# Kernel optimization log

Hardware: AMD Instinct MI355X
Metric: run time of the kernel (lower is better)

## Reference

```python
import jax, jax.numpy as jnp
import numpy as np
from math import pi as PI

N = 50000       # nodes
E = 625000      # edges
G = 64          # graphs in batch
H = 128         # hidden_channels
FLT = 128       # num_filters
NG = 50         # num_gaussians
L = 6           # num_layers
CUTOFF = 10.0
LOG2 = float(np.log(2.0))


def ssp(x):
    # ShiftedSoftplus
    return jax.nn.softplus(x) - LOG2


def setup_inputs() -> dict:
    key = jax.random.key(0)
    ks = jax.random.split(key, 20)
    xav = lambda k, shp: jax.random.normal(k, shp, jnp.float32) * jnp.sqrt(2.0 / (shp[-2] + shp[-1]))
    inp = {
        "z": jax.random.randint(ks[0], (N,), 0, 100),
        "pos": jax.random.normal(ks[1], (N, 3), jnp.float32),
        "batch": jnp.sort(jax.random.randint(ks[2], (N,), 0, G)),
        "edge_index": jax.random.randint(ks[3], (2, E), 0, N),
        "emb_table": jax.random.normal(ks[4], (100, H), jnp.float32),
        # per-layer stacked params, Linear stored as (in, out)
        "lin_W": xav(ks[5], (L, H, FLT)),
        "mlp_W1": xav(ks[6], (L, NG, FLT)),
        "mlp_b1": jnp.zeros((L, FLT), jnp.float32),
        "mlp_W2": xav(ks[7], (L, FLT, FLT)),
        "mlp_b2": jnp.zeros((L, FLT), jnp.float32),
        "v_W1": xav(ks[8], (L, FLT, H)),
        "v_b1": jnp.zeros((L, H), jnp.float32),
        "v_W2": xav(ks[9], (L, H, H)),
        "v_b2": jnp.zeros((L, H), jnp.float32),
        "u_W1": xav(ks[10], (H, H // 2)),
        "u_b1": jnp.zeros((H // 2,), jnp.float32),
        "u_W2": xav(ks[11], (H // 2, 1)),
        "u_b2": jnp.zeros((1,), jnp.float32),
    }
    return inp


def reference(z, pos, batch, edge_index, emb_table, lin_W, mlp_W1, mlp_b1,
              mlp_W2, mlp_b2, v_W1, v_b1, v_W2, v_b2, u_W1, u_b1, u_W2, u_b2):
    row, col = edge_index[0], edge_index[1]  # (j, i)
    dist = jnp.linalg.norm(pos[row] - pos[col], axis=-1)  # [E]

    # gaussian distance embedding
    offset = jnp.linspace(0.0, CUTOFF, NG)
    coeff = -0.5 / (offset[1] - offset[0]) ** 2
    dist_emb = jnp.exp(coeff * (dist[:, None] - offset[None, :]) ** 2)  # [E, NG]

    # cosine cutoff
    C = 0.5 * (jnp.cos(dist * (PI / CUTOFF)) + 1.0)  # [E]

    v = emb_table[z]  # [N, H]
    for l in range(L):
        # update_e
        W = ssp(dist_emb @ mlp_W1[l] + mlp_b1[l]) @ mlp_W2[l] + mlp_b2[l]
        W = W * C[:, None]                       # [E, F]
        e = (v @ lin_W[l])[row] * W              # gather v[j], filter multiply
        # update_v
        agg = jax.ops.segment_sum(e, col, num_segments=N)  # scatter-add to i
        out = ssp(agg @ v_W1[l] + v_b1[l]) @ v_W2[l] + v_b2[l]
        v = v + out

    # update_u readout
    h = ssp(v @ u_W1 + u_b1) @ u_W2 + u_b2       # [N, 1]
    u = jax.ops.segment_sum(h, batch, num_segments=G)  # [G, 1]
    return u
```

## Files before the change

kernel.cpp:

```cpp
#include <hip/hip_runtime.h>
#include <math.h>

#define H 128
#define NG 50
#define TB 4096
#define DMAX 12.0f
#define LOG2F_ 0.69314718055994531f

typedef __attribute__((ext_vector_type(8))) short bfrag8;
typedef __attribute__((ext_vector_type(4))) float f32x4;
typedef __attribute__((ext_vector_type(8))) unsigned short u16x8;

__device__ __forceinline__ float sspf(float x) {
    float xc = fminf(x, 60.f);
    float r = __logf(1.f + __expf(xc)) - LOG2F_;
    return r + fmaxf(x - 60.f, 0.f);
}
__device__ __forceinline__ float bf2f(unsigned short u) {
    union { unsigned int i; float f; } c; c.i = ((unsigned int)u) << 16; return c.f;
}
__device__ __forceinline__ unsigned short f2bf(float f) {
    union { float f; unsigned int i; } c; c.f = f;
    unsigned int r = c.i + 0x7fffu + ((c.i >> 16) & 1u);
    return (unsigned short)(r >> 16);
}

__global__ void embed_kernel(const int* __restrict__ z, const float* __restrict__ emb,
                             unsigned short* __restrict__ vb, int n) {
    int idx = blockIdx.x * 256 + threadIdx.x;
    if (idx < n * H) {
        int node = idx >> 7, h = idx & 127;
        vb[idx] = f2bf(emb[z[node] * H + h]);
    }
}

__global__ void prep_w_kernel(const float* __restrict__ linW, const float* __restrict__ vW1,
                              const float* __restrict__ vW2, unsigned short* __restrict__ Wt) {
    int mat = blockIdx.x >> 4;
    int local = (blockIdx.x & 15) * 256 + threadIdx.x;
    int nrow = local >> 5;
    int k4 = local & 31;
    const float* src = (mat < 6) ? linW + mat * 16384
                     : (mat < 12) ? vW1 + (mat - 6) * 16384
                                  : vW2 + (mat - 12) * 16384;
    ushort4 o;
    o.x = f2bf(src[(k4 * 4 + 0) * H + nrow]);
    o.y = f2bf(src[(k4 * 4 + 1) * H + nrow]);
    o.z = f2bf(src[(k4 * 4 + 2) * H + nrow]);
    o.w = f2bf(src[(k4 * 4 + 3) * H + nrow]);
    *(ushort4*)(Wt + mat * 16384 + nrow * H + k4 * 4) = o;
}

__global__ void prep_u_kernel(const float* __restrict__ uW1, unsigned short* __restrict__ Ut) {
    int idx = blockIdx.x * 256 + threadIdx.x;
    int c = idx >> 7, k = idx & 127;
    Ut[c * H + k] = f2bf(uW1[k * 64 + c]);
}

__global__ void edge_dist_kernel(const int* __restrict__ ei, const float* __restrict__ pos,
                                 float* __restrict__ et, int* __restrict__ deg,
                                 int E_, float inv_step) {
    int e = blockIdx.x * 256 + threadIdx.x;
    if (e >= E_) return;
    int j = ei[e];
    int i = ei[E_ + e];
    float dx = pos[j*3+0] - pos[i*3+0];
    float dy = pos[j*3+1] - pos[i*3+1];
    float dz = pos[j*3+2] - pos[i*3+2];
    float d = sqrtf(dx*dx + dy*dy + dz*dz);
    float t = d * inv_step;
    t = fminf(t, (float)(TB - 2) + 0.9999f);
    et[e] = t;
    atomicAdd(&deg[i], 1);
}

__global__ void scanA_kernel(const int* __restrict__ deg, int* __restrict__ bsum, int n) {
    __shared__ int ws[16];
    int tid = threadIdx.x;
    int idx = blockIdx.x * 1024 + tid;
    int x = (idx < n) ? deg[idx] : 0;
    #pragma unroll
    for (int off = 32; off > 0; off >>= 1) x += __shfl_xor(x, off, 64);
    int lane = tid & 63, wid = tid >> 6;
    if (lane == 0) ws[wid] = x;
    __syncthreads();
    if (tid == 0) {
        int s = 0;
        #pragma unroll
        for (int i = 0; i < 16; ++i) s += ws[i];
        bsum[blockIdx.x] = s;
    }
}

__global__ void scanB_kernel(int* __restrict__ bsum, int nb) {
    int t = threadIdx.x;
    int x = (t < nb) ? bsum[t] : 0;
    int v = x;
    #pragma unroll
    for (int off = 1; off < 64; off <<= 1) {
        int y = __shfl_up(v, off, 64);
        if (t >= off) v += y;
    }
    if (t < nb) bsum[t] = v - x;
}

__global__ void scanC_kernel(const int* __restrict__ deg, const int* __restrict__ bsum,
                             int* __restrict__ row_ptr, int* __restrict__ cursor, int n) {
    __shared__ int wsum[16];
    int tid = threadIdx.x;
    int idx = blockIdx.x * 1024 + tid;
    int lane = tid & 63, wid = tid >> 6;
    int x = (idx < n) ? deg[idx] : 0;
    int v = x;
    #pragma unroll
    for (int off = 1; off < 64; off <<= 1) {
        int y = __shfl_up(v, off, 64);
        if (lane >= off) v += y;
    }
    if (lane == 63) wsum[wid] = v;
    __syncthreads();
    int woff = 0;
    for (int w = 0; w < wid; ++w) woff += wsum[w];
    int excl = bsum[blockIdx.x] + woff + v - x;
    if (idx < n) { row_ptr[idx] = excl; cursor[idx] = excl; }
    if (idx == n - 1) row_ptr[n] = excl + x;
}

__global__ void csr_fill_kernel(const int* __restrict__ ei, const float* __restrict__ et,
                                int* __restrict__ cursor, int* __restrict__ esrc,
                                float* __restrict__ et2, int E_) {
    int e = blockIdx.x * 256 + threadIdx.x;
    if (e >= E_) return;
    int i = ei[E_ + e];
    int slot = atomicAdd(&cursor[i], 1);
    esrc[slot] = ei[e];
    et2[slot] = et[e];
}

__global__ __launch_bounds__(256) void table_all_kernel(
        const float* __restrict__ mW1, const float* __restrict__ mb1,
        const float* __restrict__ mW2, const float* __restrict__ mb2,
        unsigned short* __restrict__ tbl, float step) {
    __shared__ float gs[32][52];
    __shared__ float h1s[32][132];
    const int l = blockIdx.x >> 7;
    const int r0 = (blockIdx.x & 127) * 32;
    const float* W1 = mW1 + l * NG * H;
    const float* b1 = mb1 + l * H;
    const float* W2 = mW2 + l * H * H;
    const float* b2 = mb2 + l * H;
    const int tid = threadIdx.x;
    const float offstep = 10.0f / 49.0f;
    const float coeff = -0.5f / (offstep * offstep);

    for (int idx = tid; idx < 32 * NG; idx += 256) {
        int r = idx / NG, q = idx - r * NG;
        float dd = (r0 + r) * step - q * offstep;
        gs[r][q] = __expf(coeff * dd * dd);
    }
    __syncthreads();

    const int c = tid & 127, rb = (tid >> 7) * 16;
    {
        float acc[16];
        float bv = b1[c];
        #pragma unroll
        for (int r = 0; r < 16; ++r) acc[r] = bv;
        for (int q = 0; q < NG; ++q) {
            float w = W1[q * H + c];
            #pragma unroll
            for (int r = 0; r < 16; ++r) acc[r] = fmaf(gs[rb + r][q], w, acc[r]);
        }
        #pragma unroll
        for (int r = 0; r < 16; ++r) h1s[rb + r][c] = sspf(acc[r]);
    }
    __syncthreads();
    {
        float acc[16];
        float bv = b2[c];
        #pragma unroll
        for (int r = 0; r < 16; ++r) acc[r] = bv;
        for (int f4 = 0; f4 < 32; ++f4) {
            float w0 = W2[(f4 * 4 + 0) * H + c];
            float w1 = W2[(f4 * 4 + 1) * H + c];
            float w2 = W2[(f4 * 4 + 2) * H + c];
            float w3 = W2[(f4 * 4 + 3) * H + c];
            #pragma unroll
            for (int r = 0; r < 16; ++r) {
                float4 h = *(const float4*)&h1s[rb + r][f4 * 4];
                acc[r] = fmaf(h.x, w0, acc[r]);
                acc[r] = fmaf(h.y, w1, acc[r]);
                acc[r] = fmaf(h.z, w2, acc[r]);
                acc[r] = fmaf(h.w, w3, acc[r]);
            }
        }
        #pragma unroll
        for (int r = 0; r < 16; ++r) {
            float d = (r0 + rb + r) * step;
            float C = 0.5f * (cosf(d * 0.31415926535897932f) + 1.0f);
            tbl[(size_t)l * TB * H + (size_t)(r0 + rb + r) * H + c] = f2bf(acc[r] * C);
        }
    }
}

__global__ __launch_bounds__(256) void gemm_rs_kernel(
        const unsigned short* __restrict__ A, const unsigned short* __restrict__ Wt,
        unsigned short* __restrict__ outB, int nchunk) {
    __shared__ unsigned short t1s[4 * 16 * H];
    const int tid = threadIdx.x;
    const int task = blockIdx.x * 4 + (tid >> 6);
    if (task >= nchunk) return;
    const int lane = tid & 63, l16 = lane & 15, quad = lane >> 4;
    char* t1w = (char*)(t1s + (tid >> 6) * (16 * H));
    const size_t r0 = (size_t)task * 16;

    bfrag8 af[4];
    #pragma unroll
    for (int kc = 0; kc < 4; ++kc)
        af[kc] = *(const bfrag8*)(A + (r0 + l16) * H + (kc * 4 + quad) * 8);

    #pragma unroll
    for (int ch = 0; ch < 2; ++ch) {
        bfrag8 bf[4][4];
        f32x4 acc[4];
        #pragma unroll
        for (int nt = 0; nt < 4; ++nt) {
            #pragma unroll
            for (int kc = 0; kc < 4; ++kc)
                bf[nt][kc] = *(const bfrag8*)(Wt + (size_t)(ch * 64 + nt * 16 + l16) * H
                                              + (kc * 4 + quad) * 8);
            acc[nt] = (f32x4){0.f, 0.f, 0.f, 0.f};
        }
        #pragma unroll
        for (int nt = 0; nt < 4; ++nt)
            #pragma unroll
            for (int kc = 0; kc < 4; ++kc)
                acc[nt] = __builtin_amdgcn_mfma_f32_16x16x32_bf16(af[kc], bf[nt][kc],
                                                                  acc[nt], 0, 0, 0);
        #pragma unroll
        for (int nt = 0; nt < 4; ++nt) {
            const int col = ch * 64 + nt * 16 + l16;
            const int chunk = col >> 3;
            #pragma unroll
            for (int reg = 0; reg < 4; ++reg) {
                int m = quad * 4 + reg;
                *(unsigned short*)(t1w + m * 256 + ((chunk ^ m) * 16) + (col & 7) * 2)
                    = f2bf(acc[nt][reg]);
            }
        }
    }
    asm volatile("s_waitcnt lgkmcnt(0)" ::: "memory");
    {
        const int m = lane >> 2, cg = lane & 3;
        const size_t gr = r0 + m;
        #pragma unroll
        for (int c4 = 0; c4 < 4; ++c4) {
            int chunk = cg * 4 + c4;
            u16x8 d8 = *(const u16x8*)(t1w + m * 256 + ((chunk ^ m) * 16));
            *(u16x8*)(outB + gr * H + cg * 32 + c4 * 8) = d8;
        }
    }
}

__global__ __launch_bounds__(256, 4) void layer_kernel(
        const int* __restrict__ row_ptr, const int* __restrict__ esrc,
        const float* __restrict__ et, const unsigned short* __restrict__ tbl,
        const unsigned short* __restrict__ vlin,
        const unsigned short* __restrict__ W1t, const unsigned short* __restrict__ W2t,
        const unsigned short* __restrict__ W3t,
        const float* __restrict__ b1, const float* __restrict__ b2,
        unsigned short* __restrict__ vbf, unsigned short* __restrict__ outNext, int n) {
    __shared__ unsigned short bufA[16 * H];
    __shared__ unsigned short bufB[16 * H];
    const int tid = threadIdx.x;
    const int w = tid >> 6, lane = tid & 63;
    const int r0 = blockIdx.x * 16;
    const int l16 = lane & 15, quad = lane >> 4;

    const int rrow = tid >> 4, rcolg = tid & 15;
    const int rnode = r0 + rrow;
    u16x8 rv = {0,0,0,0,0,0,0,0};
    if (rnode < n) rv = *(const u16x8*)(vbf + (size_t)rnode * H + rcolg * 8);

    {
        const int nd = w * 4 + (lane >> 4);
        const int sub = lane & 15;
        const int node = r0 + nd;
        float acc[8] = {0.f, 0.f, 0.f, 0.f, 0.f, 0.f, 0.f, 0.f};
        if (node < n) {
            const int s = row_ptr[node], e_end = row_ptr[node + 1];
            int k = s;
            for (; k + 4 <= e_end; k += 4) {
                u16x8 w0[4], w1[4], vj[4];
                float fr[4];
                #pragma unroll
                for (int e = 0; e < 4; ++e) {
                    int j = esrc[k + e];
                    float t = et[k + e];
                    int i0 = (int)t;
                    fr[e] = t - (float)i0;
                    w0[e] = *(const u16x8*)(tbl + (size_t)i0 * H + sub * 8);
                    w1[e] = *(const u16x8*)(tbl + (size_t)i0 * H + H + sub * 8);
                    vj[e] = *(const u16x8*)(vlin + (size_t)j * H + sub * 8);
                }
                #pragma unroll
                for (int e = 0; e < 4; ++e)
                    #pragma unroll
                    for (int c = 0; c < 8; ++c) {
                        float a = bf2f(w0[e][c]);
                        acc[c] = fmaf(bf2f(vj[e][c]), fmaf(bf2f(w1[e][c]) - a, fr[e], a), acc[c]);
                    }
            }
            for (; k < e_end; ++k) {
                int j = esrc[k];
                float t = et[k];
                int i0 = (int)t;
                float fr = t - (float)i0;
                u16x8 w0v = *(const u16x8*)(tbl + (size_t)i0 * H + sub * 8);
                u16x8 w1v = *(const u16x8*)(tbl + (size_t)i0 * H + H + sub * 8);
                u16x8 vj  = *(const u16x8*)(vlin + (size_t)j * H + sub * 8);
                #pragma unroll
                for (int c = 0; c < 8; ++c) {
                    float a = bf2f(w0v[c]);
                    acc[c] = fmaf(bf2f(vj[c]), fmaf(bf2f(w1v[c]) - a, fr, a), acc[c]);
                }
            }
        }
        u16x8 o;
        #pragma unroll
        for (int c = 0; c < 8; ++c) o[c] = f2bf(acc[c]);
        *(u16x8*)((char*)bufA + nd * 256 + ((sub ^ nd) * 16)) = o;
    }
    __syncthreads();

    {
        bfrag8 af[4];
        #pragma unroll
        for (int kc = 0; kc < 4; ++kc)
            af[kc] = *(const bfrag8*)((char*)bufA + l16 * 256 + (((kc * 4 + quad) ^ l16) * 16));
        #pragma unroll
        for (int nt2 = 0; nt2 < 2; ++nt2) {
            const int colt = w * 32 + nt2 * 16;
            bfrag8 bf[4];
            #pragma unroll
            for (int kc = 0; kc < 4; ++kc)
                bf[kc] = *(const bfrag8*)(W1t + (size_t)(colt + l16) * H + (kc * 4 + quad) * 8);
            f32x4 acc = (f32x4){0.f, 0.f, 0.f, 0.f};
            #pragma unroll
            for (int kc = 0; kc < 4; ++kc)
                acc = __builtin_amdgcn_mfma_f32_16x16x32_bf16(af[kc], bf[kc], acc, 0, 0, 0);
            const int f = colt + l16;
            const float bv = b1[f];
            const int chunk = f >> 3;
            #pragma unroll
            for (int reg = 0; reg < 4; ++reg) {
                int mr = quad * 4 + reg;
                *(unsigned short*)((char*)bufB + mr * 256 + ((chunk ^ mr) * 16) + (f & 7) * 2)
                    = f2bf(sspf(acc[reg] + bv));
            }
        }
    }
    __syncthreads();

    {
        bfrag8 af[4];
        #pragma unroll
        for (int kc = 0; kc < 4; ++kc)
            af[kc] = *(const bfrag8*)((char*)bufB + l16 * 256 + (((kc * 4 + quad) ^ l16) * 16));
        #pragma unroll
        for (int nt2 = 0; nt2 < 2; ++nt2) {
            const int colt = w * 32 + nt2 * 16;
            bfrag8 bf[4];
            #pragma unroll
            for (int kc = 0; kc < 4; ++kc)
                bf[kc] = *(const bfrag8*)(W2t + (size_t)(colt + l16) * H + (kc * 4 + quad) * 8);
            f32x4 acc = (f32x4){0.f, 0.f, 0.f, 0.f};
            #pragma unroll
            for (int kc = 0; kc < 4; ++kc)
                acc = __builtin_amdgcn_mfma_f32_16x16x32_bf16(af[kc], bf[kc], acc, 0, 0, 0);
            const int col = colt + l16;
            const float bv = b2[col];
            const int chunk = col >> 3;
            #pragma unroll
            for (int reg = 0; reg < 4; ++reg) {
                int mr = quad * 4 + reg;
                *(unsigned short*)((char*)bufA + mr * 256 + ((chunk ^ mr) * 16) + (col & 7) * 2)
                    = f2bf(acc[reg] + bv);
            }
        }
    }
    __syncthreads();

    {
        u16x8 d8 = *(const u16x8*)((char*)bufA + rrow * 256 + ((rcolg ^ rrow) * 16));
        u16x8 ob;
        #pragma unroll
        for (int c = 0; c < 8; ++c) ob[c] = f2bf(bf2f(rv[c]) + bf2f(d8[c]));
        if (rnode < n) *(u16x8*)(vbf + (size_t)rnode * H + rcolg * 8) = ob;
        *(u16x8*)((char*)bufB + rrow * 256 + ((rcolg ^ rrow) * 16)) = ob;
    }
    if (!W3t) return;
    __syncthreads();

    {
        bfrag8 af[4];
        #pragma unroll
        for (int kc = 0; kc < 4; ++kc)
            af[kc] = *(const bfrag8*)((char*)bufB + l16 * 256 + (((kc * 4 + quad) ^ l16) * 16));
        #pragma unroll
        for (int nt2 = 0; nt2 < 2; ++nt2) {
            const int colt = w * 32 + nt2 * 16;
            bfrag8 bf[4];
            #pragma unroll
            for (int kc = 0; kc < 4; ++kc)
                bf[kc] = *(const bfrag8*)(W3t + (size_t)(colt + l16) * H + (kc * 4 + quad) * 8);
            f32x4 acc = (f32x4){0.f, 0.f, 0.f, 0.f};
            #pragma unroll
            for (int kc = 0; kc < 4; ++kc)
                acc = __builtin_amdgcn_mfma_f32_16x16x32_bf16(af[kc], bf[kc], acc, 0, 0, 0);
            const int col = colt + l16;
            const int chunk = col >> 3;
            #pragma unroll
            for (int reg = 0; reg < 4; ++reg) {
                int mr = quad * 4 + reg;
                *(unsigned short*)((char*)bufA + mr * 256 + ((chunk ^ mr) * 16) + (col & 7) * 2)
                    = f2bf(acc[reg]);
            }
        }
    }
    __syncthreads();
    {
        u16x8 d8 = *(const u16x8*)((char*)bufA + rrow * 256 + ((rcolg ^ rrow) * 16));
        if (rnode < n) *(u16x8*)(outNext + (size_t)rnode * H + rcolg * 8) = d8;
    }
}

__global__ __launch_bounds__(256) void readout1_kernel(
        const unsigned short* __restrict__ vbf, const unsigned short* __restrict__ Ut,
        const float* __restrict__ b1, const float* __restrict__ W2,
        const float* __restrict__ b2, const int* __restrict__ batch,
        float* __restrict__ partial, int n) {
    __shared__ unsigned short As[64 * H];
    __shared__ unsigned short Bs[64 * H];
    __shared__ float gbin[64];
    const int tid = threadIdx.x;
    const int row0 = blockIdx.x * 64;

    #pragma unroll
    for (int it = 0; it < 4; ++it) {
        int idx = it * 256 + tid;
        int r = idx >> 4, c = idx & 15;
        int gr = row0 + r;
        float4 val = (gr < n) ? *(const float4*)(vbf + (size_t)gr * H + c * 8)
                              : make_float4(0.f, 0.f, 0.f, 0.f);
        *(float4*)((char*)As + r * 256 + ((c ^ (r & 15)) * 16)) = val;
    }
    #pragma unroll
    for (int it = 0; it < 4; ++it) {
        int idx = it * 256 + tid;
        int r = idx >> 4, c = idx & 15;
        float4 val = *(const float4*)(Ut + r * H + c * 8);
        *(float4*)((char*)Bs + r * 256 + ((c ^ (r & 15)) * 16)) = val;
    }
    if (tid < 64) gbin[tid] = 0.f;
    __syncthreads();

    const int lane = tid & 63, w = tid >> 6;
    const int l16 = lane & 15, quad = lane >> 4;
    const int rA = w * 16 + l16;

    bfrag8 af[4];
    #pragma unroll
    for (int kc = 0; kc < 4; ++kc) {
        int c = kc * 4 + quad;
        af[kc] = *(const bfrag8*)((const char*)As + rA * 256 + ((c ^ (rA & 15)) * 16));
    }
    f32x4 acc[4];
    #pragma unroll
    for (int nt = 0; nt < 4; ++nt) acc[nt] = (f32x4){0.f, 0.f, 0.f, 0.f};
    #pragma unroll
    for (int nt = 0; nt < 4; ++nt) {
        const int rB = nt * 16 + l16;
        #pragma unroll
        for (int kc = 0; kc < 4; ++kc) {
            int c = kc * 4 + quad;
            bfrag8 bfr = *(const bfrag8*)((const char*)Bs + rB * 256 + ((c ^ (rB & 15)) * 16));
            acc[nt] = __builtin_amdgcn_mfma_f32_16x16x32_bf16(af[kc], bfr, acc[nt], 0, 0, 0);
        }
    }

    const float b2v = b2[0];
    float rowsum[4];
    #pragma unroll
    for (int reg = 0; reg < 4; ++reg) {
        float s = 0.f;
        #pragma unroll
        for (int nt = 0; nt < 4; ++nt) {
            int col = nt * 16 + l16;
            s += sspf(acc[nt][reg] + b1[col]) * W2[col];
        }
        s += __shfl_xor(s, 1, 64);
        s += __shfl_xor(s, 2, 64);
        s += __shfl_xor(s, 4, 64);
        s += __shfl_xor(s, 8, 64);
        rowsum[reg] = s;
    }
    if (l16 == 0) {
        #pragma unroll
        for (int reg = 0; reg < 4; ++reg) {
            int node = row0 + w * 16 + quad * 4 + reg;
            if (node < n) atomicAdd(&gbin[batch[node]], rowsum[reg] + b2v);
        }
    }
    __syncthreads();
    if (tid < 64) partial[blockIdx.x * 64 + tid] = gbin[tid];
}

__global__ void readout2_kernel(const float* __restrict__ partial, float* __restrict__ out,
                                int nb) {
    __shared__ float red[256];
    const int tid = threadIdx.x;
    const int g = tid & 63, q = tid >> 6;
    float acc = 0.f;
    for (int b = q; b < nb; b += 4) acc += partial[b * 64 + g];
    red[tid] = acc;
    __syncthreads();
    if (tid < 64) out[tid] = red[tid] + red[tid + 64] + red[tid + 128] + red[tid + 192];
}

extern "C" void kernel_launch(void* const* d_in, const int* in_sizes, int n_in,
                              void* d_out, int out_size, void* d_ws, size_t ws_size,
                              hipStream_t stream) {
    const int*   z       = (const int*)d_in[0];
    const float* pos     = (const float*)d_in[1];
    const int*   batch   = (const int*)d_in[2];
    const int*   ei      = (const int*)d_in[3];
    const float* emb     = (const float*)d_in[4];
    const float* lin_W   = (const float*)d_in[5];
    const float* mlp_W1  = (const float*)d_in[6];
    const float* mlp_b1  = (const float*)d_in[7];
    const float* mlp_W2  = (const float*)d_in[8];
    const float* mlp_b2  = (const float*)d_in[9];
    const float* v_W1    = (const float*)d_in[10];
    const float* v_b1    = (const float*)d_in[11];
    const float* v_W2    = (const float*)d_in[12];
    const float* v_b2    = (const float*)d_in[13];
    const float* u_W1    = (const float*)d_in[14];
    const float* u_b1    = (const float*)d_in[15];
    const float* u_W2    = (const float*)d_in[16];
    const float* u_b2    = (const float*)d_in[17];
    const int n  = in_sizes[0];
    const int E_ = in_sizes[3] / 2;
    float* out = (float*)d_out;

    char* wp = (char*)d_ws;
    auto alloc = [&](size_t bytes) { char* p = wp; wp += (bytes + 255) & ~(size_t)255; return p; };
    const int GB = (n + 63) / 64;
    const int NB1K = (n + 1023) / 1024;
    unsigned short* vbf     = (unsigned short*)alloc((size_t)n * H * 2);
    unsigned short* vlinA   = (unsigned short*)alloc((size_t)n * H * 2);
    unsigned short* vlinB   = (unsigned short*)alloc((size_t)n * H * 2);
    unsigned short* WtAll   = (unsigned short*)alloc((size_t)18 * H * H * 2);
    unsigned short* Ut      = (unsigned short*)alloc((size_t)64 * H * 2);
    unsigned short* tbl     = (unsigned short*)alloc((size_t)6 * TB * H * 2);
    float* et      = (float*)alloc((size_t)E_ * 4);
    float* et2     = (float*)alloc((size_t)E_ * 4);
    int*   esrc    = (int*)alloc((size_t)E_ * 4);
    int*   deg     = (int*)alloc((size_t)n * 4);
    int*   row_ptr = (int*)alloc((size_t)(n + 1) * 4);
    int*   cursor  = (int*)alloc((size_t)n * 4);
    int*   bsum    = (int*)alloc((size_t)NB1K * 4);
    float* partial = (float*)alloc((size_t)GB * 64 * 4);

    const float step = DMAX / TB;
    hipMemsetAsync(deg, 0, (size_t)n * 4, stream);
    hipMemsetAsync(out, 0, (size_t)out_size * 4, stream);

    embed_kernel<<<(n * H + 255) / 256, 256, 0, stream>>>(z, emb, vbf, n);
    prep_w_kernel<<<288, 256, 0, stream>>>(lin_W, v_W1, v_W2, WtAll);
    prep_u_kernel<<<32, 256, 0, stream>>>(u_W1, Ut);
    table_all_kernel<<<768, 256, 0, stream>>>(mlp_W1, mlp_b1, mlp_W2, mlp_b2, tbl, step);
    edge_dist_kernel<<<(E_ + 255) / 256, 256, 0, stream>>>(ei, pos, et, deg, E_, 1.0f / step);
    scanA_kernel<<<NB1K, 1024, 0, stream>>>(deg, bsum, n);
    scanB_kernel<<<1, 64, 0, stream>>>(bsum, NB1K);
    scanC_kernel<<<NB1K, 1024, 0, stream>>>(deg, bsum, row_ptr, cursor, n);
    csr_fill_kernel<<<(E_ + 255) / 256, 256, 0, stream>>>(ei, et, cursor, esrc, et2, E_);

    const int nchunk = (n + 15) / 16;
    const int GRS = (nchunk + 3) / 4;
    gemm_rs_kernel<<<GRS, 256, 0, stream>>>(vbf, WtAll, vlinA, nchunk);
    unsigned short* cur = vlinA;
    unsigned short* nxt = vlinB;
    for (int l = 0; l < 6; ++l) {
        const unsigned short* W3t = (l < 5) ? (WtAll + (l + 1) * H * H) : nullptr;
        layer_kernel<<<nchunk, 256, 0, stream>>>(row_ptr, esrc, et2,
                                                 tbl + (size_t)l * TB * H, cur,
                                                 WtAll + (6 + l) * H * H,
                                                 WtAll + (12 + l) * H * H, W3t,
                                                 v_b1 + l * H, v_b2 + l * H,
                                                 vbf, nxt, n);
        unsigned short* tmp = cur; cur = nxt; nxt = tmp;
    }
    readout1_kernel<<<GB, 256, 0, stream>>>(vbf, Ut, u_b1, u_W2, u_b2, batch, partial, n);
    readout2_kernel<<<1, 256, 0, stream>>>(partial, out, GB);
}
```

Measured before the change: 706.1 us.

## Sort nodes by degree, fuse embedding into first GEMM, halve filter table

Nodes are renumbered through a counting sort on in-degree, so the CSR row order groups nodes of similar degree. This is meant to reduce load imbalance and divergence in the per-chunk layer kernel. The embedding lookup is fused into the first GEMM, the separate scanB launch and output memset are dropped, and the filter lookup table resolution is halved to cut table build work. The permutation adds extra indirection in the readout and in the CSR fill, and the coarser table may reduce accuracy. Dropping the output memset relies on readout2 overwriting out.

```diff
diff --git a/kernel.cpp b/kernel.cpp
--- a/kernel.cpp
+++ b/kernel.cpp
@@ -3,7 +3,7 @@
 
 #define H 128
 #define NG 50
-#define TB 4096
+#define TB 2048
 #define DMAX 12.0f
 #define LOG2F_ 0.69314718055994531f
 
@@ -23,15 +23,6 @@
     union { float f; unsigned int i; } c; c.f = f;
     unsigned int r = c.i + 0x7fffu + ((c.i >> 16) & 1u);
     return (unsigned short)(r >> 16);
-}
-
-__global__ void embed_kernel(const int* __restrict__ z, const float* __restrict__ emb,
-                             unsigned short* __restrict__ vb, int n) {
-    int idx = blockIdx.x * 256 + threadIdx.x;
-    if (idx < n * H) {
-        int node = idx >> 7, h = idx & 127;
-        vb[idx] = f2bf(emb[z[node] * H + h]);
-    }
 }
 
 __global__ void prep_w_kernel(const float* __restrict__ linW, const float* __restrict__ vW1,
@@ -74,11 +65,47 @@
     atomicAdd(&deg[i], 1);
 }
 
-__global__ void scanA_kernel(const int* __restrict__ deg, int* __restrict__ bsum, int n) {
+__global__ void hist_kernel(const int* __restrict__ deg, int* __restrict__ hist, int n) {
+    __shared__ int h[64];
+    int tid = threadIdx.x;
+    if (tid < 64) h[tid] = 0;
+    __syncthreads();
+    int idx = blockIdx.x * 256 + tid;
+    if (idx < n) atomicAdd(&h[min(deg[idx], 63)], 1);
+    __syncthreads();
+    if (tid < 64 && h[tid]) atomicAdd(&hist[tid], h[tid]);
+}
+
+__global__ void histscan_kernel(const int* __restrict__ hist, int* __restrict__ cur64) {
+    int t = threadIdx.x;
+    int x = hist[t];
+    int v = x;
+    #pragma unroll
+    for (int off = 1; off < 64; off <<= 1) {
+        int y = __shfl_up(v, off, 64);
+        if (t >= off) v += y;
+    }
+    int total = __shfl(v, 63, 64);
+    cur64[t] = total - v;
+}
+
+__global__ void perm_kernel(const int* __restrict__ deg, int* __restrict__ cur64,
+                            int* __restrict__ perm, int* __restrict__ iperm,
+                            int* __restrict__ sdeg, int n) {
+    int i = blockIdx.x * 256 + threadIdx.x;
+    if (i >= n) return;
+    int d = deg[i];
+    int pos = atomicAdd(&cur64[min(d, 63)], 1);
+    perm[pos] = i;
+    iperm[i] = pos;
+    sdeg[pos] = d;
+}
+
+__global__ void scanA_kernel(const int* __restrict__ sdeg, int* __restrict__ bsum, int n) {
     __shared__ int ws[16];
     int tid = threadIdx.x;
     int idx = blockIdx.x * 1024 + tid;
-    int x = (idx < n) ? deg[idx] : 0;
+    int x = (idx < n) ? sdeg[idx] : 0;
     #pragma unroll
     for (int off = 32; off > 0; off >>= 1) x += __shfl_xor(x, off, 64);
     int lane = tid & 63, wid = tid >> 6;
@@ -92,25 +119,19 @@
     }
 }
 
-__global__ void scanB_kernel(int* __restrict__ bsum, int nb) {
-    int t = threadIdx.x;
-    int x = (t < nb) ? bsum[t] : 0;
-    int v = x;
-    #pragma unroll
-    for (int off = 1; off < 64; off <<= 1) {
-        int y = __shfl_up(v, off, 64);
-        if (t >= off) v += y;
-    }
-    if (t < nb) bsum[t] = v - x;
-}
-
-__global__ void scanC_kernel(const int* __restrict__ deg, const int* __restrict__ bsum,
+__global__ void scanC_kernel(const int* __restrict__ sdeg, const int* __restrict__ bsum,
                              int* __restrict__ row_ptr, int* __restrict__ cursor, int n) {
     __shared__ int wsum[16];
+    __shared__ int boff_s;
     int tid = threadIdx.x;
     int idx = blockIdx.x * 1024 + tid;
     int lane = tid & 63, wid = tid >> 6;
-    int x = (idx < n) ? deg[idx] : 0;
+    if (tid == 0) {
+        int s = 0;
+        for (int b = 0; b < (int)blockIdx.x; ++b) s += bsum[b];
+        boff_s = s;
+    }
+    int x = (idx < n) ? sdeg[idx] : 0;
     int v = x;
     #pragma unroll
     for (int off = 1; off < 64; off <<= 1) {
@@ -121,19 +142,20 @@
     __syncthreads();
     int woff = 0;
     for (int w = 0; w < wid; ++w) woff += wsum[w];
-    int excl = bsum[blockIdx.x] + woff + v - x;
+    int excl = boff_s + woff + v - x;
     if (idx < n) { row_ptr[idx] = excl; cursor[idx] = excl; }
     if (idx == n - 1) row_ptr[n] = excl + x;
 }
 
 __global__ void csr_fill_kernel(const int* __restrict__ ei, const float* __restrict__ et,
+                                const int* __restrict__ iperm,
                                 int* __restrict__ cursor, int* __restrict__ esrc,
                                 float* __restrict__ et2, int E_) {
     int e = blockIdx.x * 256 + threadIdx.x;
     if (e >= E_) return;
-    int i = ei[E_ + e];
-    int slot = atomicAdd(&cursor[i], 1);
-    esrc[slot] = ei[e];
+    int pi = iperm[ei[E_ + e]];
+    int slot = atomicAdd(&cursor[pi], 1);
+    esrc[slot] = iperm[ei[e]];
     et2[slot] = et[e];
 }
 
@@ -143,8 +165,8 @@
         unsigned short* __restrict__ tbl, float step) {
     __shared__ float gs[32][52];
     __shared__ float h1s[32][132];
-    const int l = blockIdx.x >> 7;
-    const int r0 = (blockIdx.x & 127) * 32;
+    const int l = blockIdx.x >> 6;
+    const int r0 = (blockIdx.x & 63) * 32;
     const float* W1 = mW1 + l * NG * H;
     const float* b1 = mb1 + l * H;
     const float* W2 = mW2 + l * H * H;
@@ -203,21 +225,32 @@
     }
 }
 
-__global__ __launch_bounds__(256) void gemm_rs_kernel(
-        const unsigned short* __restrict__ A, const unsigned short* __restrict__ Wt,
-        unsigned short* __restrict__ outB, int nchunk) {
+__global__ __launch_bounds__(256) void gemm_rs_embed_kernel(
+        const int* __restrict__ z, const int* __restrict__ perm,
+        const float* __restrict__ emb, const unsigned short* __restrict__ Wt,
+        unsigned short* __restrict__ vbf, unsigned short* __restrict__ outB, int n) {
     __shared__ unsigned short t1s[4 * 16 * H];
     const int tid = threadIdx.x;
     const int task = blockIdx.x * 4 + (tid >> 6);
-    if (task >= nchunk) return;
     const int lane = tid & 63, l16 = lane & 15, quad = lane >> 4;
     char* t1w = (char*)(t1s + (tid >> 6) * (16 * H));
     const size_t r0 = (size_t)task * 16;
-
+    const int p = (int)r0 + l16;
+    if (p >= n) return;
+
+    const float* erow = emb + (size_t)z[perm[p]] * H;
     bfrag8 af[4];
     #pragma unroll
-    for (int kc = 0; kc < 4; ++kc)
-        af[kc] = *(const bfrag8*)(A + (r0 + l16) * H + (kc * 4 + quad) * 8);
+    for (int kc = 0; kc < 4; ++kc) {
+        const int c0 = (kc * 4 + quad) * 8;
+        float4 a = *(const float4*)(erow + c0);
+        float4 b = *(const float4*)(erow + c0 + 4);
+        u16x8 o;
+        o[0] = f2bf(a.x); o[1] = f2bf(a.y); o[2] = f2bf(a.z); o[3] = f2bf(a.w);
+        o[4] = f2bf(b.x); o[5] = f2bf(b.y); o[6] = f2bf(b.z); o[7] = f2bf(b.w);
+        *(u16x8*)(vbf + (size_t)p * H + c0) = o;
+        af[kc] = (bfrag8)o;
+    }
 
     #pragma unroll
     for (int ch = 0; ch < 2; ++ch) {
@@ -439,7 +472,7 @@
         const unsigned short* __restrict__ vbf, const unsigned short* __restrict__ Ut,
         const float* __restrict__ b1, const float* __restrict__ W2,
         const float* __restrict__ b2, const int* __restrict__ batch,
-        float* __restrict__ partial, int n) {
+        const int* __restrict__ perm, float* __restrict__ partial, int n) {
     __shared__ unsigned short As[64 * H];
     __shared__ unsigned short Bs[64 * H];
     __shared__ float gbin[64];
@@ -509,7 +542,7 @@
         #pragma unroll
         for (int reg = 0; reg < 4; ++reg) {
             int node = row0 + w * 16 + quad * 4 + reg;
-            if (node < n) atomicAdd(&gbin[batch[node]], rowsum[reg] + b2v);
+            if (node < n) atomicAdd(&gbin[batch[perm[node]]], rowsum[reg] + b2v);
         }
     }
     __syncthreads();
@@ -567,28 +600,34 @@
     float* et2     = (float*)alloc((size_t)E_ * 4);
     int*   esrc    = (int*)alloc((size_t)E_ * 4);
     int*   deg     = (int*)alloc((size_t)n * 4);
+    int*   sdeg    = (int*)alloc((size_t)n * 4);
+    int*   perm    = (int*)alloc((size_t)n * 4);
+    int*   iperm   = (int*)alloc((size_t)n * 4);
     int*   row_ptr = (int*)alloc((size_t)(n + 1) * 4);
     int*   cursor  = (int*)alloc((size_t)n * 4);
     int*   bsum    = (int*)alloc((size_t)NB1K * 4);
+    int*   hist    = (int*)alloc(64 * 4);
+    int*   cur64   = (int*)alloc(64 * 4);
     float* partial = (float*)alloc((size_t)GB * 64 * 4);
 
     const float step = DMAX / TB;
     hipMemsetAsync(deg, 0, (size_t)n * 4, stream);
-    hipMemsetAsync(out, 0, (size_t)out_size * 4, stream);
-
-    embed_kernel<<<(n * H + 255) / 256, 256, 0, stream>>>(z, emb, vbf, n);
+    hipMemsetAsync(hist, 0, 64 * 4, stream);
+
     prep_w_kernel<<<288, 256, 0, stream>>>(lin_W, v_W1, v_W2, WtAll);
     prep_u_kernel<<<32, 256, 0, stream>>>(u_W1, Ut);
-    table_all_kernel<<<768, 256, 0, stream>>>(mlp_W1, mlp_b1, mlp_W2, mlp_b2, tbl, step);
+    table_all_kernel<<<384, 256, 0, stream>>>(mlp_W1, mlp_b1, mlp_W2, mlp_b2, tbl, step);
     edge_dist_kernel<<<(E_ + 255) / 256, 256, 0, stream>>>(ei, pos, et, deg, E_, 1.0f / step);
-    scanA_kernel<<<NB1K, 1024, 0, stream>>>(deg, bsum, n);
-    scanB_kernel<<<1, 64, 0, stream>>>(bsum, NB1K);
-    scanC_kernel<<<NB1K, 1024, 0, stream>>>(deg, bsum, row_ptr, cursor, n);
-    csr_fill_kernel<<<(E_ + 255) / 256, 256, 0, stream>>>(ei, et, cursor, esrc, et2, E_);
+    hist_kernel<<<(n + 255) / 256, 256, 0, stream>>>(deg, hist, n);
+    histscan_kernel<<<1, 64, 0, stream>>>(hist, cur64);
+    perm_kernel<<<(n + 255) / 256, 256, 0, stream>>>(deg, cur64, perm, iperm, sdeg, n);
+    scanA_kernel<<<NB1K, 1024, 0, stream>>>(sdeg, bsum, n);
+    scanC_kernel<<<NB1K, 1024, 0, stream>>>(sdeg, bsum, row_ptr, cursor, n);
+    csr_fill_kernel<<<(E_ + 255) / 256, 256, 0, stream>>>(ei, et, iperm, cursor, esrc, et2, E_);
 
     const int nchunk = (n + 15) / 16;
     const int GRS = (nchunk + 3) / 4;
-    gemm_rs_kernel<<<GRS, 256, 0, stream>>>(vbf, WtAll, vlinA, nchunk);
+    gemm_rs_embed_kernel<<<GRS, 256, 0, stream>>>(z, perm, emb, WtAll, vbf, vlinA, n);
     unsigned short* cur = vlinA;
     unsigned short* nxt = vlinB;
     for (int l = 0; l < 6; ++l) {
@@ -601,6 +640,6 @@
                                                  vbf, nxt, n);
         unsigned short* tmp = cur; cur = nxt; nxt = tmp;
     }
-    readout1_kernel<<<GB, 256, 0, stream>>>(vbf, Ut, u_b1, u_W2, u_b2, batch, partial, n);
+    readout1_kernel<<<GB, 256, 0, stream>>>(vbf, Ut, u_b1, u_W2, u_b2, batch, perm, partial, n);
     readout2_kernel<<<1, 256, 0, stream>>>(partial, out, GB);
 }
```

After: 799.2 us. +13.2%, slower.
